# Performance work log

Measured on AMD Instinct MI355X. Metric: run time of the kernel, lower is better.

## Reference

```python
import jax, jax.numpy as jnp
import numpy as np

N, D, B, C, T, TOD = 8192, 32, 2, 8, 12, 288
PARAM_SCALE = 0.3  # keep relu+softmax logits well-conditioned (original uses plain randn init)


def setup_inputs() -> dict:
    key = jax.random.key(0)
    k0, k1, k2, k3, k4 = jax.random.split(key, 5)
    return {
        "x": jax.random.normal(k0, (B, C, N, T), dtype=jnp.float32),
        "nodevec1": PARAM_SCALE * jax.random.normal(k1, (N, D), dtype=jnp.float32),
        "nodevec2": PARAM_SCALE * jax.random.normal(k2, (N, D), dtype=jnp.float32),
        "timevec": PARAM_SCALE * jax.random.normal(k3, (TOD, D), dtype=jnp.float32),
        "k": PARAM_SCALE * jax.random.normal(k4, (D, D, D), dtype=jnp.float32),
        "time_ind": 100,
    }


def reference(x, nodevec1, nodevec2, timevec, k, time_ind):
    # Dynamic Tucker-decomposition adjacency (SpatialGraphConv.forward, eval mode -> dropout is identity)
    tv = timevec[time_ind]                             # [D]   time_vec
    core = jnp.einsum('d,def->ef', tv, k)              # [D,D] adp1 (squeezed)
    # adp2/adp3 chain: (nodevec1 @ core) @ nodevec2.T  -> [N,N]
    adp = jnp.einsum('ne,ef->nf', nodevec1, core)      # [N,D]
    adp = jnp.einsum('nf,mf->nm', adp, nodevec2)       # [N,N]
    adp = jax.nn.softmax(jax.nn.relu(adp), axis=-1)    # row-softmax over neighbors
    # NConv: neighbor aggregation  'bcnt,nm->bcmt'
    return jnp.einsum('bcnt,nm->bcmt', x, adp)
```

## Files before the change

### kernel.cpp

```cpp
#include <hip/hip_runtime.h>
#include <hip/hip_bf16.h>


#define NN 8192
#define DD 32
#define TT 12
#define NSPLIT 8
#define CHUNK 1024
#define ESTR 72

typedef __attribute__((ext_vector_type(8))) short bf16x8;
typedef __attribute__((ext_vector_type(4))) short bf16x4;
typedef __attribute__((ext_vector_type(4))) float f32x4;

static __device__ __forceinline__ unsigned short f2bf(float f) {
  unsigned int u = __float_as_uint(f);
  u = (u + 0x7FFFu + ((u >> 16) & 1u)) >> 16;
  return (unsigned short)u;
}

static __device__ __forceinline__ float fexp2(float x) {
#if __has_builtin(__builtin_amdgcn_exp2f)
  return __builtin_amdgcn_exp2f(x);
#else
  return __builtin_exp2f(x);
#endif
}

__global__ __launch_bounds__(256) void k_prep(const float* __restrict__ nv1,
                                              const float* __restrict__ nv2,
                                              const float* __restrict__ timevec,
                                              const float* __restrict__ kk,
                                              const int* __restrict__ tind,
                                              unsigned short* __restrict__ t1b,
                                              unsigned short* __restrict__ nv2b,
                                              float* __restrict__ sums) {
  __shared__ float cs[1024];
  const int tid = threadIdx.x;
  if (tid < 128) sums[blockIdx.x * 128 + tid] = 0.f;
  const float* tv = timevec + (size_t)tind[0] * DD;
  for (int idx = tid; idx < 1024; idx += 256) {
    float acc = 0.f;
#pragma unroll
    for (int d = 0; d < DD; ++d) acc += tv[d] * kk[d * 1024 + idx];
    cs[idx] = acc;
  }
  __syncthreads();
  const int nbase = blockIdx.x * 128;
  const int f = tid & 31, sub = tid >> 5;
#pragma unroll 4
  for (int it = 0; it < 16; ++it) {
    const int n = nbase + it * 8 + sub;
    const float* nr = nv1 + (size_t)n * DD;
    float acc = 0.f;
#pragma unroll
    for (int e = 0; e < DD; ++e) acc += nr[e] * cs[e * DD + f];
    t1b[(size_t)n * DD + f] = f2bf(acc * 1.4426950408889634f);
  }
#pragma unroll 4
  for (int it = 0; it < 16; ++it) {
    const int idx = nbase * DD + it * 256 + tid;
    nv2b[idx] = f2bf(nv2[idx]);
  }
}

__global__ __launch_bounds__(256) void k_stats(const unsigned short* __restrict__ t1b,
                                               const unsigned short* __restrict__ nv2b,
                                               float* __restrict__ sums) {
  const int tid = threadIdx.x;
  const int w = tid >> 6, lane = tid & 63, q = lane >> 4, i16 = lane & 15;
  const int nbase = blockIdx.x * 64 + w * 16;
  bf16x8 a = *(const bf16x8*)(t1b + (size_t)(nbase + i16) * DD + q * 8);
  const f32x4 z4 = {0.f, 0.f, 0.f, 0.f};
  float s[4] = {0.f, 0.f, 0.f, 0.f};
  const int m0 = blockIdx.y * 1024;
  for (int mt = m0; mt < m0 + 1024; mt += 64) {
#pragma unroll
    for (int u = 0; u < 4; ++u) {
      bf16x8 b = *(const bf16x8*)(nv2b + (size_t)(mt + u * 16 + i16) * DD + q * 8);
      f32x4 d = __builtin_amdgcn_mfma_f32_16x16x32_bf16(a, b, z4, 0, 0, 0);
#pragma unroll
      for (int r = 0; r < 4; ++r) s[r] += fexp2(fmaxf(d[r], 0.f));
    }
  }
#pragma unroll
  for (int r = 0; r < 4; ++r)
    for (int off = 1; off < 16; off <<= 1) s[r] += __shfl_xor(s[r], off, 64);
  if (i16 == 0) {
#pragma unroll
    for (int r = 0; r < 4; ++r) atomicAdd(&sums[nbase + q * 4 + r], s[r]);
  }
}

__global__ __launch_bounds__(256) void k_y(const float* __restrict__ x,
                                           const float* __restrict__ sums,
                                           unsigned short* __restrict__ yT) {
  __shared__ float xs[3072];
  const int tid = threadIdx.x;
  const int n0 = blockIdx.x * 256;
  const int bc = blockIdx.y;
  const float* xp = x + (size_t)bc * NN * TT + (size_t)n0 * TT;
#pragma unroll
  for (int j = 0; j < 12; ++j) xs[j * 256 + tid] = xp[j * 256 + tid];
  __syncthreads();
  const float rinv = 1.0f / sums[n0 + tid];
#pragma unroll
  for (int t = 0; t < 12; ++t)
    yT[(size_t)(bc * TT + t) * NN + n0 + tid] = f2bf(xs[tid * 12 + t] * rinv);
}

__global__ __launch_bounds__(256, 4) void k_mega(const unsigned short* __restrict__ t1b,
                                                 const unsigned short* __restrict__ nv2b,
                                                 const unsigned short* __restrict__ yT,
                                                 float* __restrict__ part) {
  const int tid = threadIdx.x;
  const int w = tid >> 6, lane = tid & 63, q = lane >> 4, i16 = lane & 15;
  const int mb = blockIdx.x * 64;
  const int nt0 = blockIdx.y * CHUNK;

  __shared__ unsigned short Ew[2][64][ESTR];

  const bf16x8 bg = *(const bf16x8*)(nv2b + (size_t)(mb + w * 16 + i16) * DD + q * 8);
  const int rowm = w * 16 + i16;

  const f32x4 z4 = {0.f, 0.f, 0.f, 0.f};
  f32x4 acc[3][4];
#pragma unroll
  for (int c = 0; c < 3; ++c)
#pragma unroll
    for (int ms = 0; ms < 4; ++ms) acc[c][ms] = (f32x4){0.f, 0.f, 0.f, 0.f};

#pragma unroll
  for (int s = 0; s < 4; ++s) {
    bf16x8 at = *(const bf16x8*)(t1b + (size_t)(nt0 + s * 16 + i16) * DD + q * 8);
    f32x4 d = __builtin_amdgcn_mfma_f32_16x16x32_bf16(at, bg, z4, 0, 0, 0);
    bf16x4 e;
#pragma unroll
    for (int r = 0; r < 4; ++r) e[r] = (short)f2bf(fexp2(fmaxf(d[r], 0.f)));
    *(bf16x4*)&Ew[0][rowm][s * 16 + q * 4] = e;
  }
  __syncthreads();

  int p = 0;
  for (int st = 0; st < 16; ++st, p ^= 1) {
    const int nt = nt0 + st * 64;
    const bool more = (st < 15);

    bf16x8 atn[4];
    if (more) {
#pragma unroll
      for (int s = 0; s < 4; ++s)
        atn[s] = *(const bf16x8*)(t1b + (size_t)(nt + 64 + s * 16 + i16) * DD + q * 8);
    }

    bf16x8 yfr[3], efr[4];
#pragma unroll
    for (int c = 0; c < 3; ++c)
      yfr[c] = *(const bf16x8*)(yT + (size_t)((w * 3 + c) * 16 + i16) * NN + nt + q * 8);
#pragma unroll
    for (int ms = 0; ms < 4; ++ms)
      efr[ms] = *(const bf16x8*)&Ew[p][ms * 16 + i16][q * 8];

    f32x4 d0, d1;
    if (more) {
      d0 = __builtin_amdgcn_mfma_f32_16x16x32_bf16(atn[0], bg, z4, 0, 0, 0);
      d1 = __builtin_amdgcn_mfma_f32_16x16x32_bf16(atn[1], bg, z4, 0, 0, 0);
    }

#pragma unroll
    for (int c = 0; c < 3; ++c)
#pragma unroll
      for (int ms = 0; ms < 4; ++ms)
        acc[c][ms] = __builtin_amdgcn_mfma_f32_16x16x32_bf16(yfr[c], efr[ms], acc[c][ms], 0, 0, 0);

    if (more) {
      bf16x4 e0, e1;
#pragma unroll
      for (int r = 0; r < 4; ++r) {
        e0[r] = (short)f2bf(fexp2(fmaxf(d0[r], 0.f)));
        e1[r] = (short)f2bf(fexp2(fmaxf(d1[r], 0.f)));
      }
      *(bf16x4*)&Ew[p ^ 1][rowm][q * 4] = e0;
      *(bf16x4*)&Ew[p ^ 1][rowm][16 + q * 4] = e1;
      f32x4 d2 = __builtin_amdgcn_mfma_f32_16x16x32_bf16(atn[2], bg, z4, 0, 0, 0);
      f32x4 d3 = __builtin_amdgcn_mfma_f32_16x16x32_bf16(atn[3], bg, z4, 0, 0, 0);
      bf16x4 e2, e3;
#pragma unroll
      for (int r = 0; r < 4; ++r) {
        e2[r] = (short)f2bf(fexp2(fmaxf(d2[r], 0.f)));
        e3[r] = (short)f2bf(fexp2(fmaxf(d3[r], 0.f)));
      }
      *(bf16x4*)&Ew[p ^ 1][rowm][32 + q * 4] = e2;
      *(bf16x4*)&Ew[p ^ 1][rowm][48 + q * 4] = e3;
    }

#pragma unroll
    for (int c = 0; c < 3; ++c)
      yfr[c] = *(const bf16x8*)(yT + (size_t)((w * 3 + c) * 16 + i16) * NN + nt + 32 + q * 8);
#pragma unroll
    for (int ms = 0; ms < 4; ++ms)
      efr[ms] = *(const bf16x8*)&Ew[p][ms * 16 + i16][32 + q * 8];
#pragma unroll
    for (int c = 0; c < 3; ++c)
#pragma unroll
      for (int ms = 0; ms < 4; ++ms)
        acc[c][ms] = __builtin_amdgcn_mfma_f32_16x16x32_bf16(yfr[c], efr[ms], acc[c][ms], 0, 0, 0);

    __syncthreads();
  }

  float* pp = part + (size_t)blockIdx.y * 192 * NN;
#pragma unroll
  for (int c = 0; c < 3; ++c)
#pragma unroll
    for (int ms = 0; ms < 4; ++ms) {
      const int colbase = (w * 3 + c) * 16 + q * 4;
      const int m = mb + ms * 16 + i16;
#pragma unroll
      for (int r = 0; r < 4; ++r)
        pp[(size_t)(colbase + r) * NN + m] = acc[c][ms][r];
    }
}

__global__ __launch_bounds__(256) void k_reduce(const float* __restrict__ part,
                                                float* __restrict__ out) {
  __shared__ float os[3072];
  const int tid = threadIdx.x;
  const int m0 = blockIdx.x * 256;
  const int bc = blockIdx.y;
#pragma unroll
  for (int t = 0; t < 12; ++t) {
    const int col = bc * TT + t;
    float s = 0.f;
#pragma unroll
    for (int nc = 0; nc < NSPLIT; ++nc)
      s += part[((size_t)nc * 192 + col) * NN + m0 + tid];
    os[tid * 12 + t] = s;
  }
  __syncthreads();
  float* op = out + (size_t)bc * NN * TT + (size_t)m0 * TT;
#pragma unroll
  for (int j = 0; j < 12; ++j) op[j * 256 + tid] = os[j * 256 + tid];
}

extern "C" void kernel_launch(void* const* d_in, const int* in_sizes, int n_in,
                              void* d_out, int out_size, void* d_ws, size_t ws_size,
                              hipStream_t stream) {
  const float* x = (const float*)d_in[0];
  const float* nv1 = (const float*)d_in[1];
  const float* nv2 = (const float*)d_in[2];
  const float* tv = (const float*)d_in[3];
  const float* kk = (const float*)d_in[4];
  const int* tind = (const int*)d_in[5];
  float* out = (float*)d_out;

  char* ws = (char*)d_ws;
  unsigned short* t1b  = (unsigned short*)(ws);
  unsigned short* nv2b = (unsigned short*)(ws + 524288);
  float* sums          = (float*)(ws + 1048576);
  unsigned short* yT   = (unsigned short*)(ws + 1081344);
  float* part          = (float*)(ws + 4227072);

  k_prep<<<64, 256, 0, stream>>>(nv1, nv2, tv, kk, tind, t1b, nv2b, sums);
  k_stats<<<dim3(128, 8), 256, 0, stream>>>(t1b, nv2b, sums);
  k_y<<<dim3(32, 16), 256, 0, stream>>>(x, sums, yT);
  k_mega<<<dim3(128, NSPLIT), 256, 0, stream>>>(t1b, nv2b, yT, part);
  k_reduce<<<dim3(32, 16), 256, 0, stream>>>(part, out);
}
```

Measured before the change: 178.8 us.

## Compute exp adjacency tiles in registers per wave, dropping LDS staging and barriers

The main kernel no longer builds the exp(relu) adjacency tile cooperatively in shared memory with double buffering and __syncthreads. Each wave now computes all 64 columns of the tile itself in registers, using a permuted row mapping so the MFMA output layout lines up directly with the B operand of the aggregation MFMA. The aim is to remove LDS traffic, barriers and the cross-wave dependency, and it drops the occupancy hint in launch_bounds. The cost is four times the exp and MFMA work per tile, since all four waves recompute it, plus more register pressure. Separately, the transposing shared-memory buffers in k_y and k_reduce are padded to a stride of 13 to avoid bank conflicts.

```diff
diff --git a/kernel.cpp b/kernel.cpp
--- a/kernel.cpp
+++ b/kernel.cpp
@@ -7,10 +7,8 @@
 #define TT 12
 #define NSPLIT 8
 #define CHUNK 1024
-#define ESTR 72
 
 typedef __attribute__((ext_vector_type(8))) short bf16x8;
-typedef __attribute__((ext_vector_type(4))) short bf16x4;
 typedef __attribute__((ext_vector_type(4))) float f32x4;
 
 static __device__ __forceinline__ unsigned short f2bf(float f) {
@@ -26,6 +24,8 @@
   return __builtin_exp2f(x);
 #endif
 }
+
+#define MFMA32(A, B, C) __builtin_amdgcn_mfma_f32_16x16x32_bf16((A), (B), (C), 0, 0, 0)
 
 __global__ __launch_bounds__(256) void k_prep(const float* __restrict__ nv1,
                                               const float* __restrict__ nv2,
@@ -95,118 +95,92 @@
 __global__ __launch_bounds__(256) void k_y(const float* __restrict__ x,
                                            const float* __restrict__ sums,
                                            unsigned short* __restrict__ yT) {
-  __shared__ float xs[3072];
+  __shared__ float xs[3328];
   const int tid = threadIdx.x;
   const int n0 = blockIdx.x * 256;
   const int bc = blockIdx.y;
   const float* xp = x + (size_t)bc * NN * TT + (size_t)n0 * TT;
 #pragma unroll
-  for (int j = 0; j < 12; ++j) xs[j * 256 + tid] = xp[j * 256 + tid];
+  for (int j = 0; j < 12; ++j) {
+    const int idx = j * 256 + tid;
+    xs[(idx / 12) * 13 + idx % 12] = xp[idx];
+  }
   __syncthreads();
   const float rinv = 1.0f / sums[n0 + tid];
 #pragma unroll
   for (int t = 0; t < 12; ++t)
-    yT[(size_t)(bc * TT + t) * NN + n0 + tid] = f2bf(xs[tid * 12 + t] * rinv);
-}
-
-__global__ __launch_bounds__(256, 4) void k_mega(const unsigned short* __restrict__ t1b,
-                                                 const unsigned short* __restrict__ nv2b,
-                                                 const unsigned short* __restrict__ yT,
-                                                 float* __restrict__ part) {
+    yT[(size_t)(bc * TT + t) * NN + n0 + tid] = f2bf(xs[tid * 13 + t] * rinv);
+}
+
+__global__ __launch_bounds__(256) void k_mega(const unsigned short* __restrict__ t1b,
+                                              const unsigned short* __restrict__ nv2b,
+                                              const unsigned short* __restrict__ yT,
+                                              float* __restrict__ part) {
   const int tid = threadIdx.x;
   const int w = tid >> 6, lane = tid & 63, q = lane >> 4, i16 = lane & 15;
   const int mb = blockIdx.x * 64;
   const int nt0 = blockIdx.y * CHUNK;
 
-  __shared__ unsigned short Ew[2][64][ESTR];
-
-  const bf16x8 bg = *(const bf16x8*)(nv2b + (size_t)(mb + w * 16 + i16) * DD + q * 8);
-  const int rowm = w * 16 + i16;
+  bf16x8 bg[4];
+#pragma unroll
+  for (int ms = 0; ms < 4; ++ms)
+    bg[ms] = *(const bf16x8*)(nv2b + (size_t)(mb + ms * 16 + i16) * DD + q * 8);
+
+  f32x4 acc[3][4];
+#pragma unroll
+  for (int c = 0; c < 3; ++c)
+#pragma unroll
+    for (int ms = 0; ms < 4; ++ms) acc[c][ms] = (f32x4){0.f, 0.f, 0.f, 0.f};
+
+  const int perm = ((i16 >> 2) << 3) | (i16 & 3);
+  const unsigned short* tp = t1b + (size_t)(nt0 + perm) * DD + q * 8;
+  const unsigned short* yp0 = yT + (size_t)((w * 3 + 0) * 16 + i16) * NN + nt0 + q * 8;
+  const unsigned short* yp1 = yp0 + (size_t)16 * NN;
+  const unsigned short* yp2 = yp1 + (size_t)16 * NN;
+
+  bf16x8 alo = *(const bf16x8*)tp;
+  bf16x8 ahi = *(const bf16x8*)(tp + 4 * DD);
+  bf16x8 y0 = *(const bf16x8*)yp0;
+  bf16x8 y1 = *(const bf16x8*)yp1;
+  bf16x8 y2 = *(const bf16x8*)yp2;
 
   const f32x4 z4 = {0.f, 0.f, 0.f, 0.f};
-  f32x4 acc[3][4];
-#pragma unroll
-  for (int c = 0; c < 3; ++c)
-#pragma unroll
-    for (int ms = 0; ms < 4; ++ms) acc[c][ms] = (f32x4){0.f, 0.f, 0.f, 0.f};
-
-#pragma unroll
-  for (int s = 0; s < 4; ++s) {
-    bf16x8 at = *(const bf16x8*)(t1b + (size_t)(nt0 + s * 16 + i16) * DD + q * 8);
-    f32x4 d = __builtin_amdgcn_mfma_f32_16x16x32_bf16(at, bg, z4, 0, 0, 0);
-    bf16x4 e;
-#pragma unroll
-    for (int r = 0; r < 4; ++r) e[r] = (short)f2bf(fexp2(fmaxf(d[r], 0.f)));
-    *(bf16x4*)&Ew[0][rowm][s * 16 + q * 4] = e;
-  }
-  __syncthreads();
-
-  int p = 0;
-  for (int st = 0; st < 16; ++st, p ^= 1) {
-    const int nt = nt0 + st * 64;
-    const bool more = (st < 15);
-
-    bf16x8 atn[4];
-    if (more) {
-#pragma unroll
-      for (int s = 0; s < 4; ++s)
-        atn[s] = *(const bf16x8*)(t1b + (size_t)(nt + 64 + s * 16 + i16) * DD + q * 8);
-    }
-
-    bf16x8 yfr[3], efr[4];
-#pragma unroll
-    for (int c = 0; c < 3; ++c)
-      yfr[c] = *(const bf16x8*)(yT + (size_t)((w * 3 + c) * 16 + i16) * NN + nt + q * 8);
-#pragma unroll
-    for (int ms = 0; ms < 4; ++ms)
-      efr[ms] = *(const bf16x8*)&Ew[p][ms * 16 + i16][q * 8];
-
-    f32x4 d0, d1;
-    if (more) {
-      d0 = __builtin_amdgcn_mfma_f32_16x16x32_bf16(atn[0], bg, z4, 0, 0, 0);
-      d1 = __builtin_amdgcn_mfma_f32_16x16x32_bf16(atn[1], bg, z4, 0, 0, 0);
-    }
-
-#pragma unroll
-    for (int c = 0; c < 3; ++c)
-#pragma unroll
-      for (int ms = 0; ms < 4; ++ms)
-        acc[c][ms] = __builtin_amdgcn_mfma_f32_16x16x32_bf16(yfr[c], efr[ms], acc[c][ms], 0, 0, 0);
-
-    if (more) {
-      bf16x4 e0, e1;
+
+  for (int sl = 0; sl < 32; ++sl) {
+    bf16x8 alo_n, ahi_n, y0n, y1n, y2n;
+    if (sl < 31) {
+      const int o = (sl + 1) * 32;
+      alo_n = *(const bf16x8*)(tp + o * DD);
+      ahi_n = *(const bf16x8*)(tp + o * DD + 4 * DD);
+      y0n = *(const bf16x8*)(yp0 + o);
+      y1n = *(const bf16x8*)(yp1 + o);
+      y2n = *(const bf16x8*)(yp2 + o);
+    } else {
+      alo_n = alo; ahi_n = ahi; y0n = y0; y1n = y1; y2n = y2;
+    }
+
+    bf16x8 e[4];
+#pragma unroll
+    for (int ms = 0; ms < 4; ++ms) {
+      f32x4 dlo = MFMA32(alo, bg[ms], z4);
+      f32x4 dhi = MFMA32(ahi, bg[ms], z4);
+      bf16x8 t;
 #pragma unroll
       for (int r = 0; r < 4; ++r) {
-        e0[r] = (short)f2bf(fexp2(fmaxf(d0[r], 0.f)));
-        e1[r] = (short)f2bf(fexp2(fmaxf(d1[r], 0.f)));
+        t[r] = (short)f2bf(fexp2(fmaxf(dlo[r], 0.f)));
+        t[4 + r] = (short)f2bf(fexp2(fmaxf(dhi[r], 0.f)));
       }
-      *(bf16x4*)&Ew[p ^ 1][rowm][q * 4] = e0;
-      *(bf16x4*)&Ew[p ^ 1][rowm][16 + q * 4] = e1;
-      f32x4 d2 = __builtin_amdgcn_mfma_f32_16x16x32_bf16(atn[2], bg, z4, 0, 0, 0);
-      f32x4 d3 = __builtin_amdgcn_mfma_f32_16x16x32_bf16(atn[3], bg, z4, 0, 0, 0);
-      bf16x4 e2, e3;
-#pragma unroll
-      for (int r = 0; r < 4; ++r) {
-        e2[r] = (short)f2bf(fexp2(fmaxf(d2[r], 0.f)));
-        e3[r] = (short)f2bf(fexp2(fmaxf(d3[r], 0.f)));
-      }
-      *(bf16x4*)&Ew[p ^ 1][rowm][32 + q * 4] = e2;
-      *(bf16x4*)&Ew[p ^ 1][rowm][48 + q * 4] = e3;
-    }
-
-#pragma unroll
-    for (int c = 0; c < 3; ++c)
-      yfr[c] = *(const bf16x8*)(yT + (size_t)((w * 3 + c) * 16 + i16) * NN + nt + 32 + q * 8);
-#pragma unroll
-    for (int ms = 0; ms < 4; ++ms)
-      efr[ms] = *(const bf16x8*)&Ew[p][ms * 16 + i16][32 + q * 8];
-#pragma unroll
-    for (int c = 0; c < 3; ++c)
-#pragma unroll
-      for (int ms = 0; ms < 4; ++ms)
-        acc[c][ms] = __builtin_amdgcn_mfma_f32_16x16x32_bf16(yfr[c], efr[ms], acc[c][ms], 0, 0, 0);
-
-    __syncthreads();
+      e[ms] = t;
+    }
+
+#pragma unroll
+    for (int ms = 0; ms < 4; ++ms) {
+      acc[0][ms] = MFMA32(y0, e[ms], acc[0][ms]);
+      acc[1][ms] = MFMA32(y1, e[ms], acc[1][ms]);
+      acc[2][ms] = MFMA32(y2, e[ms], acc[2][ms]);
+    }
+
+    alo = alo_n; ahi = ahi_n; y0 = y0n; y1 = y1n; y2 = y2n;
   }
 
   float* pp = part + (size_t)blockIdx.y * 192 * NN;
@@ -224,7 +198,7 @@
 
 __global__ __launch_bounds__(256) void k_reduce(const float* __restrict__ part,
                                                 float* __restrict__ out) {
-  __shared__ float os[3072];
+  __shared__ float os[3328];
   const int tid = threadIdx.x;
   const int m0 = blockIdx.x * 256;
   const int bc = blockIdx.y;
@@ -235,12 +209,15 @@
 #pragma unroll
     for (int nc = 0; nc < NSPLIT; ++nc)
       s += part[((size_t)nc * 192 + col) * NN + m0 + tid];
-    os[tid * 12 + t] = s;
+    os[tid * 13 + t] = s;
   }
   __syncthreads();
   float* op = out + (size_t)bc * NN * TT + (size_t)m0 * TT;
 #pragma unroll
-  for (int j = 0; j < 12; ++j) op[j * 256 + tid] = os[j * 256 + tid];
+  for (int j = 0; j < 12; ++j) {
+    const int idx = j * 256 + tid;
+    op[idx] = os[(idx / 12) * 13 + idx % 12];
+  }
 }
 
 extern "C" void kernel_launch(void* const* d_in, const int* in_sizes, int n_in,
```

New measurement: 193.1 us. 8.0% more time.
